# Kernel tuning notes

Hardware: AMD Instinct MI355X
Metric: run time of the kernel (lower is better)

## Reference

```python
import jax, jax.numpy as jnp
import numpy as np

D_MODEL = 2048
D_FF = 4 * D_MODEL  # 8192, GPT-2 MLP convention
TOTAL = D_MODEL * D_FF          # elements per weight matrix
L = TOTAL // 2                  # complex FFT length (real/imag interleaved pairs)
NUM_COEFFS = 16
BATCH, SEQ = 2, 4096


def _decompress(coeffs_real, coeffs_imag, indices, shape, scale):
    """Faithful port of FastPoincareFourier.decompress_matrix.
    Scatter K complex coeffs into a length-L zero buffer, ifft, then
    de-interleave real/imag back into a flat real vector of length 2L == TOTAL.
    """
    coeffs = jax.lax.complex(coeffs_real, coeffs_imag)
    full_fft = jnp.zeros((L,), dtype=jnp.complex64).at[indices].set(coeffs)
    restored = jnp.fft.ifft(full_fft)  # [L] complex
    # stack([real, imag], dim=1).flatten() -> interleaved [2L]
    flat = jnp.stack([jnp.real(restored), jnp.imag(restored)], axis=1).reshape(-1)
    # 2L == TOTAL exactly (TOTAL is even), so no trunc/pad needed
    return flat.reshape(shape) * scale  # scale broadcasts ([1])


def setup_inputs() -> dict:
    key = jax.random.key(0)
    ks = jax.random.split(key, 12)
    # coefficients scaled by L*0.02 so ifft (which divides by L) yields ~N(0,0.02) weights
    cscale = L * 0.02
    return {
        "x": jax.random.normal(ks[0], (BATCH, SEQ, D_MODEL), dtype=jnp.float32),
        "fc_coeffs_real": jax.random.normal(ks[1], (NUM_COEFFS,), dtype=jnp.float32) * cscale,
        "fc_coeffs_imag": jax.random.normal(ks[2], (NUM_COEFFS,), dtype=jnp.float32) * cscale,
        "fc_scale": jax.random.uniform(ks[3], (1,), dtype=jnp.float32) + 0.5,
        "proj_coeffs_real": jax.random.normal(ks[4], (NUM_COEFFS,), dtype=jnp.float32) * cscale,
        "proj_coeffs_imag": jax.random.normal(ks[5], (NUM_COEFFS,), dtype=jnp.float32) * cscale,
        "proj_scale": jax.random.uniform(ks[6], (1,), dtype=jnp.float32) + 0.5,
        "c_fc_bias": jax.random.normal(ks[7], (D_FF,), dtype=jnp.float32) * 0.02,
        "c_proj_bias": jax.random.normal(ks[8], (D_MODEL,), dtype=jnp.float32) * 0.02,
        "fc_indices": jax.random.randint(ks[9], (NUM_COEFFS,), 0, L, dtype=jnp.int64),
        "proj_indices": jax.random.randint(ks[10], (NUM_COEFFS,), 0, L, dtype=jnp.int64),
    }


def reference(x, fc_coeffs_real, fc_coeffs_imag, fc_scale,
              proj_coeffs_real, proj_coeffs_imag, proj_scale,
              c_fc_bias, c_proj_bias, fc_indices, proj_indices):
    # W_fc: [d_model, d_ff]; F.linear(x, W.T) == x @ W
    w_fc = _decompress(fc_coeffs_real, fc_coeffs_imag, fc_indices, (D_MODEL, D_FF), fc_scale)
    h = jnp.einsum('bsd,df->bsf', x, w_fc) + c_fc_bias
    h = jax.nn.gelu(h, approximate=False)  # nn.GELU() default = exact erf
    # W_proj: [d_ff, d_model]
    w_proj = _decompress(proj_coeffs_real, proj_coeffs_imag, proj_indices, (D_FF, D_MODEL), proj_scale)
    out = jnp.einsum('bsf,fd->bsd', h, w_proj) + c_proj_bias
    return out
```

## Files before the change

kernel.cpp:

```cpp
#include <hip/hip_runtime.h>
#include <stdint.h>


typedef short bfrag8 __attribute__((ext_vector_type(8)));
typedef short bfrag4 __attribute__((ext_vector_type(4)));
typedef float f32x4  __attribute__((ext_vector_type(4)));

#define LMASK 8388607u
#define TWO_PI_OVER_L 7.4901405658478575e-7f

__device__ __forceinline__ unsigned short f2bf(float f) {
    unsigned u = __float_as_uint(f);
    u = (u + 0x7FFFu + ((u >> 16) & 1u)) >> 16;
    return (unsigned short)u;
}
__device__ __forceinline__ float bf2f(unsigned short h) {
    unsigned u = ((unsigned)h) << 16;
    return __builtin_bit_cast(float, u);
}
__device__ __forceinline__ unsigned pk2bf(float a, float b) {
    unsigned ua = __float_as_uint(a) + 0x8000u;
    unsigned ub = __float_as_uint(b) + 0x8000u;
    return __builtin_amdgcn_perm(ub, ua, 0x07060302u);
}
__device__ __forceinline__ float gelu_fast(float x) {
    float xx = x * x;
    float t  = x * fmaf(xx, -0.1029437f, -2.3022083f);
    float e  = __builtin_amdgcn_exp2f(t);
    return x * __builtin_amdgcn_rcpf(1.0f + e);
}
__device__ __forceinline__ void sc_ph(unsigned ph, float& sn, float& cs) {
    __sincosf((float)ph * TWO_PI_OVER_L, &sn, &cs);
}
__device__ __forceinline__ void rot(float& c, float& s, float cd, float sd) {
    float cn = fmaf(c, cd, -s * sd);
    s = fmaf(s, cd, c * sd);
    c = cn;
}

#if defined(__has_builtin)
#if __has_builtin(__builtin_amdgcn_mfma_f32_16x16x16bf16_1k)
#define HAVE_MFMA16_1K 1
#endif
#endif
__device__ __forceinline__ void mfma16(f32x4& acc, bfrag4 a, bfrag4 b) {
#ifdef HAVE_MFMA16_1K
    acc = __builtin_amdgcn_mfma_f32_16x16x16bf16_1k(a, b, acc, 0, 0, 0);
#else
    asm("v_mfma_f32_16x16x16_bf16 %0, %1, %2, %0" : "+v"(acc) : "v"(a), "v"(b));
#endif
}

__device__ __forceinline__ bool keep_coef(const int* __restrict__ idx, int kk) {
    int v = idx[kk];
    bool keep = true;
    for (int j = kk + 1; j < 16; ++j) keep = keep && (idx[j] != v);
    return keep;
}

__global__ __launch_bounds__(512, 4) void k_t1(
    const float* __restrict__ x,
    const float* __restrict__ fcr, const float* __restrict__ fci,
    const int* __restrict__ fidx,  const float* __restrict__ fcs,
    unsigned short* __restrict__ t1)
{
    __shared__ float red[8 * 512];
    const int tid  = threadIdx.x;
    const int w    = tid >> 6;
    const int lane = tid & 63;
    const int lr   = lane & 15;
    const int hi   = lane >> 4;
    const size_t tok0 = (size_t)blockIdx.x * 16;

    const float sc = fcs[0] * (1.0f / 8388608.0f);
    const int p   = lr & 1;
    const int kk0 = lr >> 1, kk1 = 8 + (lr >> 1);
    unsigned s0, s1; float a0, b0, a1, b1;
    {
        bool k0 = keep_coef(fidx, kk0), k1 = keep_coef(fidx, kk1);
        s0 = (((unsigned)fidx[kk0]) << 12) & LMASK;
        s1 = (((unsigned)fidx[kk1]) << 12) & LMASK;
        a0 = k0 ? fcr[kk0] * sc : 0.f;  b0 = k0 ? fci[kk0] * sc : 0.f;
        a1 = k1 ? fcr[kk1] * sc : 0.f;  b1 = k1 ? fci[kk1] * sc : 0.f;
    }
    const float al0 = p ? b0 : a0, be0 = p ? a0 : -b0;
    const float al1 = p ? b1 : a1, be1 = p ? a1 : -b1;
    float c1r0, s1r0, c32r0, s32r0, cse0, sse0;
    float c1r1, s1r1, c32r1, s32r1, cse1, sse1;
    {
        const unsigned kb = (unsigned)(w * 256 + hi * 8);
        float sn, cs_;
        sc_ph(s0, sn, cs_);                    c1r0 = cs_;  s1r0 = sn;
        sc_ph((s0 * 32u) & LMASK, sn, cs_);    c32r0 = cs_; s32r0 = sn;
        sc_ph((s0 * kb) & LMASK, sn, cs_);     cse0 = cs_;  sse0 = sn;
        sc_ph(s1, sn, cs_);                    c1r1 = cs_;  s1r1 = sn;
        sc_ph((s1 * 32u) & LMASK, sn, cs_);    c32r1 = cs_; s32r1 = sn;
        sc_ph((s1 * kb) & LMASK, sn, cs_);     cse1 = cs_;  sse1 = sn;
    }

    f32x4 acc[2];
    { f32x4 z = {0.f,0.f,0.f,0.f}; acc[0] = z; acc[1] = z; }
    #pragma unroll 2
    for (int s = 0; s < 8; ++s) {
        int k = w * 256 + s * 32 + hi * 8;
        const float* xp = x + (tok0 + lr) * 2048 + k;
        float4 v0 = *(const float4*)xp;
        float4 v1 = *(const float4*)(xp + 4);
        uint4 aw = make_uint4(pk2bf(v0.x, v0.y), pk2bf(v0.z, v0.w),
                              pk2bf(v1.x, v1.y), pk2bf(v1.z, v1.w));
        bfrag8 af = __builtin_bit_cast(bfrag8, aw);
        float e0[8], e1[8];
        {
            float c = cse0, s_ = sse0;
            #pragma unroll
            for (int t = 0; t < 8; ++t) {
                e0[t] = fmaf(al0, c, be0 * s_);
                if (t < 7) rot(c, s_, c1r0, s1r0);
            }
            rot(cse0, sse0, c32r0, s32r0);
        }
        {
            float c = cse1, s_ = sse1;
            #pragma unroll
            for (int t = 0; t < 8; ++t) {
                e1[t] = fmaf(al1, c, be1 * s_);
                if (t < 7) rot(c, s_, c1r1, s1r1);
            }
            rot(cse1, sse1, c32r1, s32r1);
        }
        uint4 bw0 = make_uint4(pk2bf(e0[0], e0[1]), pk2bf(e0[2], e0[3]),
                               pk2bf(e0[4], e0[5]), pk2bf(e0[6], e0[7]));
        uint4 bw1 = make_uint4(pk2bf(e1[0], e1[1]), pk2bf(e1[2], e1[3]),
                               pk2bf(e1[4], e1[5]), pk2bf(e1[6], e1[7]));
        bfrag8 bf0 = __builtin_bit_cast(bfrag8, bw0);
        bfrag8 bf1 = __builtin_bit_cast(bfrag8, bw1);
        acc[0] = __builtin_amdgcn_mfma_f32_16x16x32_bf16(af, bf0, acc[0], 0, 0, 0);
        acc[1] = __builtin_amdgcn_mfma_f32_16x16x32_bf16(af, bf1, acc[1], 0, 0, 0);
    }
    #pragma unroll
    for (int nj = 0; nj < 2; ++nj)
        #pragma unroll
        for (int r = 0; r < 4; ++r)
            red[w * 512 + (hi * 4 + r) * 32 + nj * 16 + lr] = acc[nj][r];
    __syncthreads();
    float s = 0.f;
    #pragma unroll
    for (int w2 = 0; w2 < 8; ++w2) s += red[w2 * 512 + tid];
    t1[(size_t)blockIdx.x * 512 + tid] = f2bf(s);
}

__global__ __launch_bounds__(512, 4) void k_mid(
    const unsigned short* __restrict__ t1,
    const int* __restrict__ fidx,
    const int* __restrict__ pidx,
    const float* __restrict__ prr, const float* __restrict__ pri,
    const float* __restrict__ prs,
    const float* __restrict__ fcb,
    unsigned short* __restrict__ t2p)
{
    __shared__ __align__(16) unsigned short vfc[512 * 40];
    __shared__ __align__(16) unsigned short upr[32 * 520];
    __shared__ float lbias[512];
    const int tid  = threadIdx.x;
    const int w    = tid >> 6;
    const int lane = tid & 63;
    const int lr   = lane & 15;
    const int hi   = lane >> 4;
    const int fc   = blockIdx.x;

    {
        int jg = fc * 512 + tid;
        unsigned m = ((unsigned)jg) >> 1;
        int pj = jg & 1;
        unsigned short* row = vfc + tid * 40;
        #pragma unroll
        for (int k = 0; k < 16; ++k) {
            float sn, cs;
            sc_ph(((((unsigned)fidx[k]) & LMASK) * m) & LMASK, sn, cs);
            row[2 * k]     = f2bf(pj ? sn : cs);
            row[2 * k + 1] = f2bf(pj ? cs : -sn);
        }
    }
    {
        const float scp = prs[0] * (1.0f / 8388608.0f);
        int k  = tid >> 5;
        int f0 = (tid & 31) * 16;
        bool kp = keep_coef(pidx, k);
        unsigned s = (((unsigned)pidx[k]) << 10) & LMASK;
        float a = kp ? prr[k] * scp : 0.f;
        float b = kp ? pri[k] * scp : 0.f;
        unsigned short* r0 = upr + (2 * k) * 520 + f0;
        unsigned short* r1 = upr + (2 * k + 1) * 520 + f0;
        unsigned fg = (unsigned)(fc * 512 + f0);
        #pragma unroll
        for (int t = 0; t < 16; ++t) {
            float sn, cs;
            sc_ph((s * (fg + t)) & LMASK, sn, cs);
            r0[t] = f2bf(fmaf(a, cs, -b * sn));
            r1[t] = f2bf(fmaf(a, sn, b * cs));
        }
    }
    lbias[tid] = fcb[fc * 512 + tid];
    __syncthreads();

    const int ga = blockIdx.y * 16 + w * 2, gb = ga + 1;
    const int toff = lr * 32 + hi * 8;
    const bfrag8 tA = *(const bfrag8*)(t1 + (size_t)ga * 512 + toff);
    const bfrag8 tB = *(const bfrag8*)(t1 + (size_t)gb * 512 + toff);
    f32x4 aA0[2], aA1[2], aB0[2], aB1[2];
    #pragma unroll
    for (int h = 0; h < 2; ++h) {
        f32x4 z = {0.f,0.f,0.f,0.f};
        aA0[h] = z; aA1[h] = z; aB0[h] = z; aB1[h] = z;
    }

    #pragma unroll 2
    for (int it = 0; it < 16; ++it) {
        const int f0 = it * 32;
        bfrag8 va0 = *(const bfrag8*)(vfc + (f0 + lr) * 40 + hi * 8);
        bfrag8 va1 = *(const bfrag8*)(vfc + (f0 + 16 + lr) * 40 + hi * 8);
        f32x4 cb0 = *(const f32x4*)(lbias + f0 + hi * 4);
        f32x4 cb1 = *(const f32x4*)(lbias + f0 + 16 + hi * 4);
        bfrag4 u00 = *(const bfrag4*)(upr + lr * 520 + f0 + hi * 4);
        bfrag4 u10 = *(const bfrag4*)(upr + (16 + lr) * 520 + f0 + hi * 4);
        bfrag4 u01 = *(const bfrag4*)(upr + lr * 520 + f0 + 16 + hi * 4);
        bfrag4 u11 = *(const bfrag4*)(upr + (16 + lr) * 520 + f0 + 16 + hi * 4);
        f32x4 sA0 = __builtin_amdgcn_mfma_f32_16x16x32_bf16(va0, tA, cb0, 0, 0, 0);
        f32x4 sB0 = __builtin_amdgcn_mfma_f32_16x16x32_bf16(va0, tB, cb0, 0, 0, 0);
        f32x4 sA1 = __builtin_amdgcn_mfma_f32_16x16x32_bf16(va1, tA, cb1, 0, 0, 0);
        f32x4 sB1 = __builtin_amdgcn_mfma_f32_16x16x32_bf16(va1, tB, cb1, 0, 0, 0);
        uint2 hA0 = make_uint2(pk2bf(gelu_fast(sA0[0]), gelu_fast(sA0[1])),
                               pk2bf(gelu_fast(sA0[2]), gelu_fast(sA0[3])));
        uint2 hB0 = make_uint2(pk2bf(gelu_fast(sB0[0]), gelu_fast(sB0[1])),
                               pk2bf(gelu_fast(sB0[2]), gelu_fast(sB0[3])));
        uint2 hA1 = make_uint2(pk2bf(gelu_fast(sA1[0]), gelu_fast(sA1[1])),
                               pk2bf(gelu_fast(sA1[2]), gelu_fast(sA1[3])));
        uint2 hB1 = make_uint2(pk2bf(gelu_fast(sB1[0]), gelu_fast(sB1[1])),
                               pk2bf(gelu_fast(sB1[2]), gelu_fast(sB1[3])));
        bfrag4 fA0 = __builtin_bit_cast(bfrag4, hA0);
        bfrag4 fB0 = __builtin_bit_cast(bfrag4, hB0);
        bfrag4 fA1 = __builtin_bit_cast(bfrag4, hA1);
        bfrag4 fB1 = __builtin_bit_cast(bfrag4, hB1);
        mfma16(aA0[0], u00, fA0);
        mfma16(aA1[0], u10, fA0);
        mfma16(aB0[0], u00, fB0);
        mfma16(aB1[0], u10, fB0);
        mfma16(aA0[1], u01, fA1);
        mfma16(aA1[1], u11, fA1);
        mfma16(aB0[1], u01, fB1);
        mfma16(aB1[1], u11, fB1);
    }
    f32x4 vA0 = aA0[0] + aA0[1], vA1 = aA1[0] + aA1[1];
    f32x4 vB0 = aB0[0] + aB0[1], vB1 = aB1[0] + aB1[1];

    {
        unsigned short* oa = t2p + ((size_t)fc * 512 + ga) * 512;
        unsigned short* ob = t2p + ((size_t)fc * 512 + gb) * 512;
        *(uint2*)(oa + lr * 32 + hi * 4)      = make_uint2(pk2bf(vA0[0], vA0[1]), pk2bf(vA0[2], vA0[3]));
        *(uint2*)(oa + lr * 32 + 16 + hi * 4) = make_uint2(pk2bf(vA1[0], vA1[1]), pk2bf(vA1[2], vA1[3]));
        *(uint2*)(ob + lr * 32 + hi * 4)      = make_uint2(pk2bf(vB0[0], vB0[1]), pk2bf(vB0[2], vB0[3]));
        *(uint2*)(ob + lr * 32 + 16 + hi * 4) = make_uint2(pk2bf(vB1[0], vB1[1]), pk2bf(vB1[2], vB1[3]));
    }
}

__global__ __launch_bounds__(512, 4) void k_out(
    const unsigned short* __restrict__ t2p,
    const int* __restrict__ pidx,
    const float* __restrict__ prb,
    float* __restrict__ out)
{
    __shared__ unsigned short lT[512];
    const int tid  = threadIdx.x;
    const int w    = tid >> 6;
    const int lane = tid & 63;
    const int lr   = lane & 15;
    const int hi   = lane >> 4;
    const int g    = blockIdx.x;
    const size_t tok0 = (size_t)g * 16;

    {
        float s = 0.f;
        #pragma unroll
        for (int c = 0; c < 16; ++c)
            s += bf2f(t2p[((size_t)c * 512 + g) * 512 + tid]);
        lT[tid] = f2bf(s);
    }
    const int pd = lr & 1;
    float rc0, rs0, rc1, rs1, rc2, rs2, rc3, rs3;
    float dc0, ds0, dc1, ds1, dc2, ds2, dc3, ds3;
    {
        unsigned m0 = (unsigned)(w * 128 + (lr >> 1));
        float sn, cs_;
        unsigned k0 = ((unsigned)pidx[hi * 4 + 0]) & LMASK;
        unsigned k1 = ((unsigned)pidx[hi * 4 + 1]) & LMASK;
        unsigned k2 = ((unsigned)pidx[hi * 4 + 2]) & LMASK;
        unsigned k3 = ((unsigned)pidx[hi * 4 + 3]) & LMASK;
        sc_ph((k0 * m0) & LMASK, sn, cs_); rc0 = cs_; rs0 = sn;
        sc_ph((k0 * 8u) & LMASK, sn, cs_); dc0 = cs_; ds0 = sn;
        sc_ph((k1 * m0) & LMASK, sn, cs_); rc1 = cs_; rs1 = sn;
        sc_ph((k1 * 8u) & LMASK, sn, cs_); dc1 = cs_; ds1 = sn;
        sc_ph((k2 * m0) & LMASK, sn, cs_); rc2 = cs_; rs2 = sn;
        sc_ph((k2 * 8u) & LMASK, sn, cs_); dc2 = cs_; ds2 = sn;
        sc_ph((k3 * m0) & LMASK, sn, cs_); rc3 = cs_; rs3 = sn;
        sc_ph((k3 * 8u) & LMASK, sn, cs_); dc3 = cs_; ds3 = sn;
    }
    __syncthreads();
    const bfrag8 t2a = *(const bfrag8*)(lT + lr * 32 + hi * 8);
    #pragma unroll 4
    for (int nj = 0; nj < 16; ++nj) {
        int d = w * 256 + nj * 16 + lr;
        float v0 = pd ? rs0 : rc0, v1 = pd ? rc0 : -rs0;
        float v2 = pd ? rs1 : rc1, v3 = pd ? rc1 : -rs1;
        float v4 = pd ? rs2 : rc2, v5 = pd ? rc2 : -rs2;
        float v6 = pd ? rs3 : rc3, v7 = pd ? rc3 : -rs3;
        uint4 pw = make_uint4(pk2bf(v0, v1), pk2bf(v2, v3),
                              pk2bf(v4, v5), pk2bf(v6, v7));
        bfrag8 vp = __builtin_bit_cast(bfrag8, pw);
        float bn = prb[d];
        f32x4 c4 = {bn, bn, bn, bn};
        f32x4 o = __builtin_amdgcn_mfma_f32_16x16x32_bf16(t2a, vp, c4, 0, 0, 0);
        #pragma unroll
        for (int r = 0; r < 4; ++r)
            out[(tok0 + hi * 4 + r) * 2048 + d] = o[r];
        rot(rc0, rs0, dc0, ds0);
        rot(rc1, rs1, dc1, ds1);
        rot(rc2, rs2, dc2, ds2);
        rot(rc3, rs3, dc3, ds3);
    }
}

extern "C" void kernel_launch(void* const* d_in, const int* in_sizes, int n_in,
                              void* d_out, int out_size, void* d_ws, size_t ws_size,
                              hipStream_t stream) {
    (void)in_sizes; (void)n_in; (void)out_size; (void)ws_size;
    const float* x   = (const float*)d_in[0];
    const float* fcr = (const float*)d_in[1];
    const float* fci = (const float*)d_in[2];
    const float* fcs = (const float*)d_in[3];
    const float* prr = (const float*)d_in[4];
    const float* pri = (const float*)d_in[5];
    const float* prs = (const float*)d_in[6];
    const float* fcb = (const float*)d_in[7];
    const float* prb = (const float*)d_in[8];
    const int* fidx  = (const int*)d_in[9];
    const int* pidx  = (const int*)d_in[10];
    float* out = (float*)d_out;
    char* ws = (char*)d_ws;

    size_t off = 0;
    auto take = [&](size_t bytes) { size_t p = off; off = (off + bytes + 255) & ~(size_t)255; return p; };
    unsigned short* t1  = (unsigned short*)(ws + take((size_t)8192 * 32 * 2));
    unsigned short* t2p = (unsigned short*)(ws + take((size_t)16 * 8192 * 32 * 2));

    k_t1 <<<dim3(512),    512, 0, stream>>>(x, fcr, fci, fidx, fcs, t1);
    k_mid<<<dim3(16, 32), 512, 0, stream>>>(t1, fidx, pidx, prr, pri, prs, fcb, t2p);
    k_out<<<dim3(512),    512, 0, stream>>>(t2p, pidx, prb, out);
}
```

Before: 62.80 us.

## Split k_mid d_ff chunk to 256 for more blocks and higher occupancy

Halves the d_ff slice each k_mid block handles, from 512 to 256, and doubles the grid along that axis to 32x32. Shared-memory basis tables shrink accordingly and the two setup tables are now built by separate halves of the block, which allows launch bounds of 8 blocks per CU. The aim is better latency hiding and CU fill for the mid-stage GEMM. In exchange the partial-sum buffer has twice as many chunks, so k_out reads and reduces 32 partials instead of 16 per token group, and the inner loop drops its two-way unroll.

```diff
diff --git a/kernel.cpp b/kernel.cpp
--- a/kernel.cpp
+++ b/kernel.cpp
@@ -149,7 +149,7 @@
     t1[(size_t)blockIdx.x * 512 + tid] = f2bf(s);
 }
 
-__global__ __launch_bounds__(512, 4) void k_mid(
+__global__ __launch_bounds__(512, 8) void k_mid(
     const unsigned short* __restrict__ t1,
     const int* __restrict__ fidx,
     const int* __restrict__ pidx,
@@ -158,9 +158,9 @@
     const float* __restrict__ fcb,
     unsigned short* __restrict__ t2p)
 {
-    __shared__ __align__(16) unsigned short vfc[512 * 40];
-    __shared__ __align__(16) unsigned short upr[32 * 520];
-    __shared__ float lbias[512];
+    __shared__ __align__(16) unsigned short vfc[256 * 40];
+    __shared__ __align__(16) unsigned short upr[32 * 264];
+    __shared__ float lbias[256];
     const int tid  = threadIdx.x;
     const int w    = tid >> 6;
     const int lane = tid & 63;
@@ -168,8 +168,8 @@
     const int hi   = lane >> 4;
     const int fc   = blockIdx.x;
 
-    {
-        int jg = fc * 512 + tid;
+    if (tid < 256) {
+        int jg = fc * 256 + tid;
         unsigned m = ((unsigned)jg) >> 1;
         int pj = jg & 1;
         unsigned short* row = vfc + tid * 40;
@@ -180,18 +180,19 @@
             row[2 * k]     = f2bf(pj ? sn : cs);
             row[2 * k + 1] = f2bf(pj ? cs : -sn);
         }
-    }
-    {
+        lbias[tid] = fcb[fc * 256 + tid];
+    } else {
         const float scp = prs[0] * (1.0f / 8388608.0f);
-        int k  = tid >> 5;
-        int f0 = (tid & 31) * 16;
+        int idx = tid - 256;
+        int k  = idx >> 4;
+        int f0 = (idx & 15) * 16;
         bool kp = keep_coef(pidx, k);
         unsigned s = (((unsigned)pidx[k]) << 10) & LMASK;
         float a = kp ? prr[k] * scp : 0.f;
         float b = kp ? pri[k] * scp : 0.f;
-        unsigned short* r0 = upr + (2 * k) * 520 + f0;
-        unsigned short* r1 = upr + (2 * k + 1) * 520 + f0;
-        unsigned fg = (unsigned)(fc * 512 + f0);
+        unsigned short* r0 = upr + (2 * k) * 264 + f0;
+        unsigned short* r1 = upr + (2 * k + 1) * 264 + f0;
+        unsigned fg = (unsigned)(fc * 256 + f0);
         #pragma unroll
         for (int t = 0; t < 16; ++t) {
             float sn, cs;
@@ -200,66 +201,43 @@
             r1[t] = f2bf(fmaf(a, sn, b * cs));
         }
     }
-    lbias[tid] = fcb[fc * 512 + tid];
     __syncthreads();
 
     const int ga = blockIdx.y * 16 + w * 2, gb = ga + 1;
     const int toff = lr * 32 + hi * 8;
     const bfrag8 tA = *(const bfrag8*)(t1 + (size_t)ga * 512 + toff);
     const bfrag8 tB = *(const bfrag8*)(t1 + (size_t)gb * 512 + toff);
-    f32x4 aA0[2], aA1[2], aB0[2], aB1[2];
-    #pragma unroll
-    for (int h = 0; h < 2; ++h) {
-        f32x4 z = {0.f,0.f,0.f,0.f};
-        aA0[h] = z; aA1[h] = z; aB0[h] = z; aB1[h] = z;
-    }
-
-    #pragma unroll 2
+    f32x4 aA0 = {0.f,0.f,0.f,0.f}, aA1 = {0.f,0.f,0.f,0.f};
+    f32x4 aB0 = {0.f,0.f,0.f,0.f}, aB1 = {0.f,0.f,0.f,0.f};
+
+    #pragma unroll 1
     for (int it = 0; it < 16; ++it) {
-        const int f0 = it * 32;
-        bfrag8 va0 = *(const bfrag8*)(vfc + (f0 + lr) * 40 + hi * 8);
-        bfrag8 va1 = *(const bfrag8*)(vfc + (f0 + 16 + lr) * 40 + hi * 8);
-        f32x4 cb0 = *(const f32x4*)(lbias + f0 + hi * 4);
-        f32x4 cb1 = *(const f32x4*)(lbias + f0 + 16 + hi * 4);
-        bfrag4 u00 = *(const bfrag4*)(upr + lr * 520 + f0 + hi * 4);
-        bfrag4 u10 = *(const bfrag4*)(upr + (16 + lr) * 520 + f0 + hi * 4);
-        bfrag4 u01 = *(const bfrag4*)(upr + lr * 520 + f0 + 16 + hi * 4);
-        bfrag4 u11 = *(const bfrag4*)(upr + (16 + lr) * 520 + f0 + 16 + hi * 4);
-        f32x4 sA0 = __builtin_amdgcn_mfma_f32_16x16x32_bf16(va0, tA, cb0, 0, 0, 0);
-        f32x4 sB0 = __builtin_amdgcn_mfma_f32_16x16x32_bf16(va0, tB, cb0, 0, 0, 0);
-        f32x4 sA1 = __builtin_amdgcn_mfma_f32_16x16x32_bf16(va1, tA, cb1, 0, 0, 0);
-        f32x4 sB1 = __builtin_amdgcn_mfma_f32_16x16x32_bf16(va1, tB, cb1, 0, 0, 0);
-        uint2 hA0 = make_uint2(pk2bf(gelu_fast(sA0[0]), gelu_fast(sA0[1])),
-                               pk2bf(gelu_fast(sA0[2]), gelu_fast(sA0[3])));
-        uint2 hB0 = make_uint2(pk2bf(gelu_fast(sB0[0]), gelu_fast(sB0[1])),
-                               pk2bf(gelu_fast(sB0[2]), gelu_fast(sB0[3])));
-        uint2 hA1 = make_uint2(pk2bf(gelu_fast(sA1[0]), gelu_fast(sA1[1])),
-                               pk2bf(gelu_fast(sA1[2]), gelu_fast(sA1[3])));
-        uint2 hB1 = make_uint2(pk2bf(gelu_fast(sB1[0]), gelu_fast(sB1[1])),
-                               pk2bf(gelu_fast(sB1[2]), gelu_fast(sB1[3])));
-        bfrag4 fA0 = __builtin_bit_cast(bfrag4, hA0);
-        bfrag4 fB0 = __builtin_bit_cast(bfrag4, hB0);
-        bfrag4 fA1 = __builtin_bit_cast(bfrag4, hA1);
-        bfrag4 fB1 = __builtin_bit_cast(bfrag4, hB1);
-        mfma16(aA0[0], u00, fA0);
-        mfma16(aA1[0], u10, fA0);
-        mfma16(aB0[0], u00, fB0);
-        mfma16(aB1[0], u10, fB0);
-        mfma16(aA0[1], u01, fA1);
-        mfma16(aA1[1], u11, fA1);
-        mfma16(aB0[1], u01, fB1);
-        mfma16(aB1[1], u11, fB1);
-    }
-    f32x4 vA0 = aA0[0] + aA0[1], vA1 = aA1[0] + aA1[1];
-    f32x4 vB0 = aB0[0] + aB0[1], vB1 = aB1[0] + aB1[1];
+        const int f0 = it * 16;
+        bfrag8 va = *(const bfrag8*)(vfc + (f0 + lr) * 40 + hi * 8);
+        f32x4 cb = *(const f32x4*)(lbias + f0 + hi * 4);
+        bfrag4 u0 = *(const bfrag4*)(upr + lr * 264 + f0 + hi * 4);
+        bfrag4 u1 = *(const bfrag4*)(upr + (16 + lr) * 264 + f0 + hi * 4);
+        f32x4 sA = __builtin_amdgcn_mfma_f32_16x16x32_bf16(va, tA, cb, 0, 0, 0);
+        f32x4 sB = __builtin_amdgcn_mfma_f32_16x16x32_bf16(va, tB, cb, 0, 0, 0);
+        uint2 hwA = make_uint2(pk2bf(gelu_fast(sA[0]), gelu_fast(sA[1])),
+                               pk2bf(gelu_fast(sA[2]), gelu_fast(sA[3])));
+        uint2 hwB = make_uint2(pk2bf(gelu_fast(sB[0]), gelu_fast(sB[1])),
+                               pk2bf(gelu_fast(sB[2]), gelu_fast(sB[3])));
+        bfrag4 hA = __builtin_bit_cast(bfrag4, hwA);
+        bfrag4 hB = __builtin_bit_cast(bfrag4, hwB);
+        mfma16(aA0, u0, hA);
+        mfma16(aA1, u1, hA);
+        mfma16(aB0, u0, hB);
+        mfma16(aB1, u1, hB);
+    }
 
     {
         unsigned short* oa = t2p + ((size_t)fc * 512 + ga) * 512;
         unsigned short* ob = t2p + ((size_t)fc * 512 + gb) * 512;
-        *(uint2*)(oa + lr * 32 + hi * 4)      = make_uint2(pk2bf(vA0[0], vA0[1]), pk2bf(vA0[2], vA0[3]));
-        *(uint2*)(oa + lr * 32 + 16 + hi * 4) = make_uint2(pk2bf(vA1[0], vA1[1]), pk2bf(vA1[2], vA1[3]));
-        *(uint2*)(ob + lr * 32 + hi * 4)      = make_uint2(pk2bf(vB0[0], vB0[1]), pk2bf(vB0[2], vB0[3]));
-        *(uint2*)(ob + lr * 32 + 16 + hi * 4) = make_uint2(pk2bf(vB1[0], vB1[1]), pk2bf(vB1[2], vB1[3]));
+        *(uint2*)(oa + lr * 32 + hi * 4)      = make_uint2(pk2bf(aA0[0], aA0[1]), pk2bf(aA0[2], aA0[3]));
+        *(uint2*)(oa + lr * 32 + 16 + hi * 4) = make_uint2(pk2bf(aA1[0], aA1[1]), pk2bf(aA1[2], aA1[3]));
+        *(uint2*)(ob + lr * 32 + hi * 4)      = make_uint2(pk2bf(aB0[0], aB0[1]), pk2bf(aB0[2], aB0[3]));
+        *(uint2*)(ob + lr * 32 + 16 + hi * 4) = make_uint2(pk2bf(aB1[0], aB1[1]), pk2bf(aB1[2], aB1[3]));
     }
 }
 
@@ -281,7 +259,7 @@
     {
         float s = 0.f;
         #pragma unroll
-        for (int c = 0; c < 16; ++c)
+        for (int c = 0; c < 32; ++c)
             s += bf2f(t2p[((size_t)c * 512 + g) * 512 + tid]);
         lT[tid] = f2bf(s);
     }
@@ -350,9 +328,9 @@
     size_t off = 0;
     auto take = [&](size_t bytes) { size_t p = off; off = (off + bytes + 255) & ~(size_t)255; return p; };
     unsigned short* t1  = (unsigned short*)(ws + take((size_t)8192 * 32 * 2));
-    unsigned short* t2p = (unsigned short*)(ws + take((size_t)16 * 8192 * 32 * 2));
+    unsigned short* t2p = (unsigned short*)(ws + take((size_t)32 * 512 * 512 * 2));
 
     k_t1 <<<dim3(512),    512, 0, stream>>>(x, fcr, fci, fidx, fcs, t1);
-    k_mid<<<dim3(16, 32), 512, 0, stream>>>(t1, fidx, pidx, prr, pri, prs, fcb, t2p);
+    k_mid<<<dim3(32, 32), 512, 0, stream>>>(t1, fidx, pidx, prr, pri, prs, fcb, t2p);
     k_out<<<dim3(512),    512, 0, stream>>>(t2p, pidx, prb, out);
 }
```

After: 63.52 us. About the same (+1.1%).
